# Performance work log

Measured on AMD Instinct MI355X. Metric: run time of the kernel, lower is better.

## Reference

```python
import jax, jax.numpy as jnp
import numpy as np

N_EMBD = 768
N_HEAD = 8
HEAD_DIM = N_EMBD // N_HEAD


def setup_inputs() -> dict:
    key = jax.random.key(0)
    k1, k2, k3 = jax.random.split(key, 3)
    B, T, C = 8, 1024, N_EMBD
    x = jax.random.normal(k1, (B, T, C), dtype=jnp.float32)
    # nn.Linear(C, 3C, bias=False): store as [C, 3C] so y = x @ W
    W_attn = jax.random.normal(k2, (C, 3 * C), dtype=jnp.float32) * (1.0 / np.sqrt(C))
    W_proj = jax.random.normal(k3, (C, C), dtype=jnp.float32) * (1.0 / np.sqrt(C))
    return {"x": x, "W_attn": W_attn, "W_proj": W_proj}


def reference(x, W_attn, W_proj):
    B, T, C = x.shape
    qkv = x @ W_attn                      # [B,T,3C]
    q, k, v = jnp.split(qkv, 3, axis=2)
    # [B,T,C] -> [B,H,T,D]
    def heads(t):
        return t.reshape(B, T, N_HEAD, HEAD_DIM).transpose(0, 2, 1, 3)
    q, k, v = heads(q), heads(k), heads(v)
    scale = 1.0 / np.sqrt(HEAD_DIM)
    att = jnp.einsum('bhtd,bhsd->bhts', q, k) * scale  # [B,H,T,T]
    causal = jnp.tril(jnp.ones((T, T), dtype=bool))
    att = jnp.where(causal[None, None], att, -jnp.inf)
    att = jax.nn.softmax(att, axis=-1)
    y = jnp.einsum('bhts,bhsd->bhtd', att, v)          # [B,H,T,D]
    y = y.transpose(0, 2, 1, 3).reshape(B, T, C)
    return y @ W_proj
```

## Files before the change

kernel.cpp:

```cpp
#include <hip/hip_runtime.h>
#include <stdint.h>

#define Bz 8
#define Tz 1024
#define Cz 768
#define Hz 8
#define Dz 96
#define BHz 64
#define Kz 768

typedef __bf16 bf16x8 __attribute__((ext_vector_type(8)));
typedef unsigned short u16x8 __attribute__((ext_vector_type(8)));
typedef float f32x4 __attribute__((ext_vector_type(4)));

__device__ __forceinline__ unsigned short f2bf(float f) {
  union { float f; unsigned int u; } v; v.f = f;
  unsigned int u = v.u;
  return (unsigned short)((u + 0x7fffu + ((u >> 16) & 1u)) >> 16);
}

__device__ __forceinline__ unsigned int cvtpk(float a, float b) {
  unsigned int r;
  asm("v_cvt_pk_bf16_f32 %0, %1, %2" : "=v"(r) : "v"(a), "v"(b));
  return r;
}

#if defined(__has_builtin)
#if __has_builtin(__builtin_amdgcn_exp2f)
#define EXP2(x) __builtin_amdgcn_exp2f(x)
#endif
#endif
#ifndef EXP2
#define EXP2(x) __expf((x) * 0.6931471805599453f)
#endif

typedef const __attribute__((address_space(1))) void* gas_ptr;
typedef __attribute__((address_space(3))) void* las_ptr;
__device__ __forceinline__ void gl16(const void* g, void* l) {
  __builtin_amdgcn_global_load_lds((gas_ptr)g, (las_ptr)l, 16, 0, 0);
}

__global__ __launch_bounds__(256) void prep(const float* __restrict__ x,
                                            unsigned short* __restrict__ xb,
                                            const float* __restrict__ Wa,
                                            unsigned short* __restrict__ Wat,
                                            const float* __restrict__ Wp,
                                            unsigned short* __restrict__ Wpt) {
  __shared__ unsigned short t[64][72];
  const int bid = blockIdx.x;
  const int tid = threadIdx.x;
  if (bid < 6144) {
    int i = (bid * 256 + tid) * 4;
    float4 v = *(const float4*)(x + i);
    union { unsigned short s[4]; uint2 u; } o;
    o.s[0] = f2bf(v.x); o.s[1] = f2bf(v.y); o.s[2] = f2bf(v.z); o.s[3] = f2bf(v.w);
    *(uint2*)(xb + i) = o.u;
    return;
  }
  const float* in; unsigned short* out; int R, Cc, bx, by;
  if (bid < 6576) { int q = bid - 6144; in = Wa; out = Wat; R = 768; Cc = 2304; bx = (q % 36) * 64; by = (q / 36) * 64; }
  else            { int q = bid - 6576; in = Wp; out = Wpt; R = 768; Cc = 768;  bx = (q % 12) * 64; by = (q / 12) * 64; }
#pragma unroll
  for (int i = 0; i < 16; i++) {
    int idx = tid + i * 256;
    int r = idx >> 6, c = idx & 63;
    t[c][r] = f2bf(in[(by + r) * Cc + bx + c]);
  }
  __syncthreads();
#pragma unroll
  for (int i = 0; i < 16; i++) {
    int idx = tid + i * 256;
    int r = idx >> 6, c = idx & 63;
    out[(bx + r) * R + by + c] = t[r][c];
  }
}

template <int MODE>
__global__ __launch_bounds__(256)
void gemm128(const unsigned short* __restrict__ A,
             const unsigned short* __restrict__ Bt,
             unsigned short* __restrict__ obf,
             float* __restrict__ of32) {
  __shared__ unsigned short Asm[2][128 * 32];
  __shared__ unsigned short Bsm[2][128 * 32];
  const int tid = threadIdx.x;
  const int wave = tid >> 6, lane = tid & 63;
  const int quad = lane >> 4, l16 = lane & 15;
  const int bm = blockIdx.x, bn = blockIdx.y;
  const int wm = (wave >> 1) * 64, wn = (wave & 1) * 64;

  f32x4 zero = {0.f, 0.f, 0.f, 0.f};
  f32x4 acc[4][4];
#pragma unroll
  for (int i = 0; i < 4; i++)
#pragma unroll
    for (int j = 0; j < 4; j++) acc[i][j] = zero;

  const int sch = (lane & 3) ^ ((lane >> 3) & 3);
  const unsigned short* Agp = A + (size_t)(bm * 128 + wave * 16 + (lane >> 2)) * Kz + sch * 8;
  const unsigned short* Bgp = Bt + (size_t)(bn * 128 + wave * 16 + (lane >> 2)) * Kz + sch * 8;
  const int ldst = (wave * 16) * 32;

#pragma unroll
  for (int g = 0; g < 2; g++) {
    gl16(Agp + g * 64 * Kz, &Asm[0][g * 2048 + ldst]);
    gl16(Bgp + g * 64 * Kz, &Bsm[0][g * 2048 + ldst]);
  }
  __syncthreads();

  const int rc = (quad ^ ((l16 >> 1) & 3)) << 3;
  int cur = 0;
  for (int t = 0; t < Kz / 32; t++) {
    if (t + 1 < Kz / 32) {
      const int kn = (t + 1) * 32;
#pragma unroll
      for (int g = 0; g < 2; g++) {
        gl16(Agp + g * 64 * Kz + kn, &Asm[cur ^ 1][g * 2048 + ldst]);
        gl16(Bgp + g * 64 * Kz + kn, &Bsm[cur ^ 1][g * 2048 + ldst]);
      }
    }
    bf16x8 af[4], bfr[4];
#pragma unroll
    for (int mi = 0; mi < 4; mi++)
      af[mi] = *(const bf16x8*)&Asm[cur][(wm + mi * 16 + l16) * 32 + rc];
#pragma unroll
    for (int ni = 0; ni < 4; ni++)
      bfr[ni] = *(const bf16x8*)&Bsm[cur][(wn + ni * 16 + l16) * 32 + rc];
#pragma unroll
    for (int mi = 0; mi < 4; mi++)
#pragma unroll
      for (int ni = 0; ni < 4; ni++)
        acc[mi][ni] = __builtin_amdgcn_mfma_f32_16x16x32_bf16(af[mi], bfr[ni], acc[mi][ni], 0, 0, 0);
    __syncthreads();
    cur ^= 1;
  }

#pragma unroll
  for (int mi = 0; mi < 4; mi++) {
    int row = bm * 128 + wm + mi * 16 + quad * 4;
    if (MODE == 0) {
      int b = row >> 10;
      int t = row & 1023;
#pragma unroll
      for (int ni = 0; ni < 4; ni++) {
        int col = bn * 128 + wn + ni * 16 + l16;
        int which = col / 768;
        int cc = col - which * 768;
        int h = cc / 96;
        int d = cc - h * 96;
        if (which == 2) {
          int tp = (t & ~31) | (((t >> 2) & 3) << 3) | (((t >> 4) & 1) << 2) | (t & 3);
          int base = ((2 * 64 + b * 8 + h) * 96 + d) * 1024 + tp;
          union { unsigned short s[4]; uint2 u; } o;
#pragma unroll
          for (int r = 0; r < 4; r++) o.s[r] = f2bf(acc[mi][ni][r]);
          *(uint2*)(obf + base) = o.u;
        } else {
          int base = ((which * 64 + b * 8 + h) * 1024 + t) * 96 + d;
#pragma unroll
          for (int r = 0; r < 4; r++) obf[base + r * 96] = f2bf(acc[mi][ni][r]);
        }
      }
    } else {
#pragma unroll
      for (int ni = 0; ni < 4; ni++) {
        int col = bn * 128 + wn + ni * 16 + l16;
#pragma unroll
        for (int r = 0; r < 4; r++) of32[(row + r) * 768 + col] = acc[mi][ni][r];
      }
    }
  }
}

__global__ __launch_bounds__(256, 4)
void attn(const unsigned short* __restrict__ qkv, unsigned short* __restrict__ y) {
  const int bh = blockIdx.x;
  const int by = blockIdx.y;
  const int q0 = (15 - by) * 64;
  const int tid = threadIdx.x;
  const int wave = tid >> 6, lane = tid & 63;
  const int quad = lane >> 4, l16 = lane & 15;
  const int qw0 = q0 + wave * 16;
  const int b = bh >> 3, h = bh & 7;

  const unsigned short* Qh = qkv + bh * Tz * Dz;
  const unsigned short* Kh = qkv + (BHz + bh) * Tz * Dz;
  const unsigned short* Vt = qkv + 2 * BHz * Tz * Dz + bh * Dz * Tz;

  __shared__ unsigned short Vsm[96 * 128];

  bf16x8 aq[3];
#pragma unroll
  for (int kd = 0; kd < 3; kd++)
    aq[kd] = *(const bf16x8*)(Qh + (qw0 + l16) * Dz + kd * 32 + quad * 8);

  f32x4 zero = {0.f, 0.f, 0.f, 0.f};
  f32x4 acc_o[6];
#pragma unroll
  for (int i = 0; i < 6; i++) acc_o[i] = zero;
  const float NEG = -__builtin_inff();
  float lrow = 0.f;
  const float cs = 0.14724538519872735f;
  const int t_abs = qw0 + l16;

  const int vrow = wave * 24 + (lane >> 4);
  const int vch = lane & 15;

  const int s_last = (q0 >> 7) << 7;
  for (int s0 = 0; s0 <= s_last; s0 += 128) {
    __syncthreads();
#pragma unroll
    for (int g = 0; g < 6; g++) {
      const int row = vrow + g * 4;
      gl16(Vt + row * Tz + s0 + ((vch ^ (row & 7)) << 3),
           &Vsm[(wave * 24 + g * 4) * 128]);
    }

    const int srem = qw0 + 15 - s0;
    const int nlim = min(7, srem >> 4);
    const int klim = min(3, srem >> 5);

    f32x4 sacc[8];
#pragma unroll
    for (int ni = 0; ni < 8; ni++) {
      if (ni <= nlim) {
        sacc[ni] = zero;
#pragma unroll
        for (int kd = 0; kd < 3; kd++) {
          bf16x8 bk = *(const bf16x8*)(Kh + (s0 + ni * 16 + l16) * Dz + kd * 32 + quad * 8);
          sacc[ni] = __builtin_amdgcn_mfma_f32_16x16x32_bf16(bk, aq[kd], sacc[ni], 0, 0, 0);
        }
      }
    }

#pragma unroll
    for (int ni = 0; ni < 8; ni++) {
      if (ni <= nlim && s0 + ni * 16 + 15 > qw0) {
        const int s_base = s0 + ni * 16 + quad * 4;
#pragma unroll
        for (int r = 0; r < 4; r++)
          if (s_base + r > t_abs) sacc[ni][r] = NEG;
      }
    }

    float rs[4] = {0.f, 0.f, 0.f, 0.f};
    unsigned int pk[8][2];
#pragma unroll
    for (int ni = 0; ni < 8; ni++) {
      if (ni <= nlim) {
        float p0 = EXP2(sacc[ni][0] * cs);
        float p1 = EXP2(sacc[ni][1] * cs);
        float p2 = EXP2(sacc[ni][2] * cs);
        float p3 = EXP2(sacc[ni][3] * cs);
        rs[0] += p0; rs[1] += p1; rs[2] += p2; rs[3] += p3;
        pk[ni][0] = cvtpk(p0, p1);
        pk[ni][1] = cvtpk(p2, p3);
      } else {
        pk[ni][0] = 0u; pk[ni][1] = 0u;
      }
    }
    lrow += (rs[0] + rs[1]) + (rs[2] + rs[3]);

    __syncthreads();

#pragma unroll
    for (int kc = 0; kc < 4; kc++) {
      if (kc <= klim) {
        union { unsigned int w[4]; bf16x8 v; } ap;
        ap.w[0] = pk[2 * kc][0];
        ap.w[1] = pk[2 * kc][1];
        ap.w[2] = pk[2 * kc + 1][0];
        ap.w[3] = pk[2 * kc + 1][1];
#pragma unroll
        for (int di = 0; di < 6; di++) {
          bf16x8 bv = *(const bf16x8*)&Vsm[(di * 16 + l16) * 128 +
                                           (((kc * 4 + quad) ^ (l16 & 7)) << 3)];
          acc_o[di] = __builtin_amdgcn_mfma_f32_16x16x32_bf16(ap.v, bv, acc_o[di], 0, 0, 0);
        }
      }
    }
  }

  lrow += __shfl_xor(lrow, 16);
  lrow += __shfl_xor(lrow, 32);
  float linv = 1.f / lrow;
  float lv[4];
#pragma unroll
  for (int r = 0; r < 4; r++) lv[r] = __shfl(linv, quad * 4 + r);
#pragma unroll
  for (int r = 0; r < 4; r++) {
    int t = qw0 + quad * 4 + r;
#pragma unroll
    for (int di = 0; di < 6; di++) {
      int d = di * 16 + l16;
      y[(b * Tz + t) * Cz + h * Dz + d] = f2bf(acc_o[di][r] * lv[r]);
    }
  }
}

#define OFF_XB   0u
#define OFF_WAT  12582912u
#define OFF_WPT  16121856u
#define OFF_QKV  17301504u
#define OFF_Y    55050240u

extern "C" void kernel_launch(void* const* d_in, const int* in_sizes, int n_in,
                              void* d_out, int out_size, void* d_ws, size_t ws_size,
                              hipStream_t stream) {
  const float* x  = (const float*)d_in[0];
  const float* Wa = (const float*)d_in[1];
  const float* Wp = (const float*)d_in[2];
  float* out = (float*)d_out;
  uint8_t* ws = (uint8_t*)d_ws;
  unsigned short* xb  = (unsigned short*)(ws + OFF_XB);
  unsigned short* Wat = (unsigned short*)(ws + OFF_WAT);
  unsigned short* Wpt = (unsigned short*)(ws + OFF_WPT);
  unsigned short* qkv = (unsigned short*)(ws + OFF_QKV);
  unsigned short* y   = (unsigned short*)(ws + OFF_Y);

  prep<<<6720, 256, 0, stream>>>(x, xb, Wa, Wat, Wp, Wpt);
  gemm128<0><<<dim3(64, 18), 256, 0, stream>>>(xb, Wat, qkv, nullptr);
  attn<<<dim3(64, 16), 256, 0, stream>>>(qkv, y);
  gemm128<1><<<dim3(64, 6), 256, 0, stream>>>(y, Wpt, nullptr, out);
}
```

Before: 198.7 us.

## Fuse x bf16 conversion into QKV GEMM, shrink output GEMM tile, reorder attention blocks

The QKV GEMM now reads fp32 x directly, converts it to bf16 in registers and stores it into swizzled LDS. This removes the separate conversion pass and its 12 MB intermediate buffer. The output projection GEMM moves to a 64-row tile, doubling the grid to 768 blocks for better CU fill. Attention query blocks are dispatched in an interleaved order so long and short causal rows mix across the grid. The cost is that every QKV block column re-reads and re-converts x in fp32 (18 times), which adds global traffic and register use.

```diff
diff --git a/kernel.cpp b/kernel.cpp
--- a/kernel.cpp
+++ b/kernel.cpp
@@ -40,26 +40,16 @@
   __builtin_amdgcn_global_load_lds((gas_ptr)g, (las_ptr)l, 16, 0, 0);
 }
 
-__global__ __launch_bounds__(256) void prep(const float* __restrict__ x,
-                                            unsigned short* __restrict__ xb,
-                                            const float* __restrict__ Wa,
+__global__ __launch_bounds__(256) void prep(const float* __restrict__ Wa,
                                             unsigned short* __restrict__ Wat,
                                             const float* __restrict__ Wp,
                                             unsigned short* __restrict__ Wpt) {
   __shared__ unsigned short t[64][72];
   const int bid = blockIdx.x;
   const int tid = threadIdx.x;
-  if (bid < 6144) {
-    int i = (bid * 256 + tid) * 4;
-    float4 v = *(const float4*)(x + i);
-    union { unsigned short s[4]; uint2 u; } o;
-    o.s[0] = f2bf(v.x); o.s[1] = f2bf(v.y); o.s[2] = f2bf(v.z); o.s[3] = f2bf(v.w);
-    *(uint2*)(xb + i) = o.u;
-    return;
-  }
   const float* in; unsigned short* out; int R, Cc, bx, by;
-  if (bid < 6576) { int q = bid - 6144; in = Wa; out = Wat; R = 768; Cc = 2304; bx = (q % 36) * 64; by = (q / 36) * 64; }
-  else            { int q = bid - 6576; in = Wp; out = Wpt; R = 768; Cc = 768;  bx = (q % 12) * 64; by = (q / 12) * 64; }
+  if (bid < 432) { int q = bid;       in = Wa; out = Wat; R = 768; Cc = 2304; bx = (q % 36) * 64; by = (q / 36) * 64; }
+  else           { int q = bid - 432; in = Wp; out = Wpt; R = 768; Cc = 768;  bx = (q % 12) * 64; by = (q / 12) * 64; }
 #pragma unroll
   for (int i = 0; i < 16; i++) {
     int idx = tid + i * 256;
@@ -75,12 +65,10 @@
   }
 }
 
-template <int MODE>
 __global__ __launch_bounds__(256)
-void gemm128(const unsigned short* __restrict__ A,
-             const unsigned short* __restrict__ Bt,
-             unsigned short* __restrict__ obf,
-             float* __restrict__ of32) {
+void gemm_qkv(const float* __restrict__ x,
+              const unsigned short* __restrict__ Bt,
+              unsigned short* __restrict__ obf) {
   __shared__ unsigned short Asm[2][128 * 32];
   __shared__ unsigned short Bsm[2][128 * 32];
   const int tid = threadIdx.x;
@@ -96,16 +84,115 @@
 #pragma unroll
     for (int j = 0; j < 4; j++) acc[i][j] = zero;
 
+  const int ar = tid >> 1, ah = tid & 1;
+  const float* xg = x + (size_t)(bm * 128 + ar) * Kz + ah * 16;
+  const int s4 = (ar >> 1) & 3;
+  const int ca = ((2 * ah) ^ s4) << 3;
+  const int cb = ((2 * ah + 1) ^ s4) << 3;
+
   const int sch = (lane & 3) ^ ((lane >> 3) & 3);
-  const unsigned short* Agp = A + (size_t)(bm * 128 + wave * 16 + (lane >> 2)) * Kz + sch * 8;
   const unsigned short* Bgp = Bt + (size_t)(bn * 128 + wave * 16 + (lane >> 2)) * Kz + sch * 8;
   const int ldst = (wave * 16) * 32;
 
-#pragma unroll
-  for (int g = 0; g < 2; g++) {
-    gl16(Agp + g * 64 * Kz, &Asm[0][g * 2048 + ldst]);
-    gl16(Bgp + g * 64 * Kz, &Bsm[0][g * 2048 + ldst]);
-  }
+  float4 xv0, xv1, xv2, xv3;
+#define LOADX(K) { xv0 = *(const float4*)(xg + (K));      xv1 = *(const float4*)(xg + (K) + 4); \
+                   xv2 = *(const float4*)(xg + (K) + 8);  xv3 = *(const float4*)(xg + (K) + 12); }
+#define STOREA(B) { uint4 da = { cvtpk(xv0.x, xv0.y), cvtpk(xv0.z, xv0.w),                      \
+                                 cvtpk(xv1.x, xv1.y), cvtpk(xv1.z, xv1.w) };                    \
+                    uint4 db = { cvtpk(xv2.x, xv2.y), cvtpk(xv2.z, xv2.w),                      \
+                                 cvtpk(xv3.x, xv3.y), cvtpk(xv3.z, xv3.w) };                    \
+                    *(uint4*)&Asm[B][ar * 32 + ca] = da;                                        \
+                    *(uint4*)&Asm[B][ar * 32 + cb] = db; }
+
+  LOADX(0);
+#pragma unroll
+  for (int g = 0; g < 2; g++) gl16(Bgp + g * 64 * Kz, &Bsm[0][g * 2048 + ldst]);
+  STOREA(0);
+  __syncthreads();
+
+  const int rc = (quad ^ ((l16 >> 1) & 3)) << 3;
+  int cur = 0;
+  for (int t = 0; t < Kz / 32; t++) {
+    const int nxt = (t + 1) * 32;
+    if (t + 1 < Kz / 32) {
+      LOADX(nxt);
+#pragma unroll
+      for (int g = 0; g < 2; g++) gl16(Bgp + g * 64 * Kz + nxt, &Bsm[cur ^ 1][g * 2048 + ldst]);
+    }
+    bf16x8 af[4], bfr[4];
+#pragma unroll
+    for (int mi = 0; mi < 4; mi++)
+      af[mi] = *(const bf16x8*)&Asm[cur][(wm + mi * 16 + l16) * 32 + rc];
+#pragma unroll
+    for (int ni = 0; ni < 4; ni++)
+      bfr[ni] = *(const bf16x8*)&Bsm[cur][(wn + ni * 16 + l16) * 32 + rc];
+#pragma unroll
+    for (int mi = 0; mi < 4; mi++)
+#pragma unroll
+      for (int ni = 0; ni < 4; ni++)
+        acc[mi][ni] = __builtin_amdgcn_mfma_f32_16x16x32_bf16(af[mi], bfr[ni], acc[mi][ni], 0, 0, 0);
+    if (t + 1 < Kz / 32) STOREA(cur ^ 1);
+    __syncthreads();
+    cur ^= 1;
+  }
+
+#pragma unroll
+  for (int mi = 0; mi < 4; mi++) {
+    int row = bm * 128 + wm + mi * 16 + quad * 4;
+    int b = row >> 10;
+    int t = row & 1023;
+#pragma unroll
+    for (int ni = 0; ni < 4; ni++) {
+      int col = bn * 128 + wn + ni * 16 + l16;
+      int which = col / 768;
+      int cc = col - which * 768;
+      int h = cc / 96;
+      int d = cc - h * 96;
+      if (which == 2) {
+        int tp = (t & ~31) | (((t >> 2) & 3) << 3) | (((t >> 4) & 1) << 2) | (t & 3);
+        int base = ((2 * 64 + b * 8 + h) * 96 + d) * 1024 + tp;
+        union { unsigned short s[4]; uint2 u; } o;
+#pragma unroll
+        for (int r = 0; r < 4; r++) o.s[r] = f2bf(acc[mi][ni][r]);
+        *(uint2*)(obf + base) = o.u;
+      } else {
+        int base = ((which * 64 + b * 8 + h) * 1024 + t) * 96 + d;
+#pragma unroll
+        for (int r = 0; r < 4; r++) obf[base + r * 96] = f2bf(acc[mi][ni][r]);
+      }
+    }
+  }
+#undef LOADX
+#undef STOREA
+}
+
+__global__ __launch_bounds__(256)
+void gemm_out(const unsigned short* __restrict__ A,
+              const unsigned short* __restrict__ Bt,
+              float* __restrict__ of32) {
+  __shared__ unsigned short Asm[2][64 * 32];
+  __shared__ unsigned short Bsm[2][128 * 32];
+  const int tid = threadIdx.x;
+  const int wave = tid >> 6, lane = tid & 63;
+  const int quad = lane >> 4, l16 = lane & 15;
+  const int bm = blockIdx.x, bn = blockIdx.y;
+  const int wm = (wave >> 1) * 32, wn = (wave & 1) * 64;
+
+  f32x4 zero = {0.f, 0.f, 0.f, 0.f};
+  f32x4 acc[2][4];
+#pragma unroll
+  for (int i = 0; i < 2; i++)
+#pragma unroll
+    for (int j = 0; j < 4; j++) acc[i][j] = zero;
+
+  const int sch = (lane & 3) ^ ((lane >> 3) & 3);
+  const unsigned short* Agp = A + (size_t)(bm * 64 + wave * 16 + (lane >> 2)) * Kz + sch * 8;
+  const unsigned short* Bgp = Bt + (size_t)(bn * 128 + wave * 16 + (lane >> 2)) * Kz + sch * 8;
+  const int ldst = (wave * 16) * 32;
+
+  gl16(Agp, &Asm[0][ldst]);
+#pragma unroll
+  for (int g = 0; g < 2; g++) gl16(Bgp + g * 64 * Kz, &Bsm[0][g * 2048 + ldst]);
   __syncthreads();
 
   const int rc = (quad ^ ((l16 >> 1) & 3)) << 3;
@@ -113,21 +200,19 @@
   for (int t = 0; t < Kz / 32; t++) {
     if (t + 1 < Kz / 32) {
       const int kn = (t + 1) * 32;
-#pragma unroll
-      for (int g = 0; g < 2; g++) {
-        gl16(Agp + g * 64 * Kz + kn, &Asm[cur ^ 1][g * 2048 + ldst]);
-        gl16(Bgp + g * 64 * Kz + kn, &Bsm[cur ^ 1][g * 2048 + ldst]);
-      }
-    }
-    bf16x8 af[4], bfr[4];
-#pragma unroll
-    for (int mi = 0; mi < 4; mi++)
+      gl16(Agp + kn, &Asm[cur ^ 1][ldst]);
+#pragma unroll
+      for (int g = 0; g < 2; g++) gl16(Bgp + g * 64 * Kz + kn, &Bsm[cur ^ 1][g * 2048 + ldst]);
+    }
+    bf16x8 af[2], bfr[4];
+#pragma unroll
+    for (int mi = 0; mi < 2; mi++)
       af[mi] = *(const bf16x8*)&Asm[cur][(wm + mi * 16 + l16) * 32 + rc];
 #pragma unroll
     for (int ni = 0; ni < 4; ni++)
       bfr[ni] = *(const bf16x8*)&Bsm[cur][(wn + ni * 16 + l16) * 32 + rc];
 #pragma unroll
-    for (int mi = 0; mi < 4; mi++)
+    for (int mi = 0; mi < 2; mi++)
 #pragma unroll
       for (int ni = 0; ni < 4; ni++)
         acc[mi][ni] = __builtin_amdgcn_mfma_f32_16x16x32_bf16(af[mi], bfr[ni], acc[mi][ni], 0, 0, 0);
@@ -136,38 +221,13 @@
   }
 
 #pragma unroll
-  for (int mi = 0; mi < 4; mi++) {
-    int row = bm * 128 + wm + mi * 16 + quad * 4;
-    if (MODE == 0) {
-      int b = row >> 10;
-      int t = row & 1023;
-#pragma unroll
-      for (int ni = 0; ni < 4; ni++) {
-        int col = bn * 128 + wn + ni * 16 + l16;
-        int which = col / 768;
-        int cc = col - which * 768;
-        int h = cc / 96;
-        int d = cc - h * 96;
-        if (which == 2) {
-          int tp = (t & ~31) | (((t >> 2) & 3) << 3) | (((t >> 4) & 1) << 2) | (t & 3);
-          int base = ((2 * 64 + b * 8 + h) * 96 + d) * 1024 + tp;
-          union { unsigned short s[4]; uint2 u; } o;
-#pragma unroll
-          for (int r = 0; r < 4; r++) o.s[r] = f2bf(acc[mi][ni][r]);
-          *(uint2*)(obf + base) = o.u;
-        } else {
-          int base = ((which * 64 + b * 8 + h) * 1024 + t) * 96 + d;
-#pragma unroll
-          for (int r = 0; r < 4; r++) obf[base + r * 96] = f2bf(acc[mi][ni][r]);
-        }
-      }
-    } else {
-#pragma unroll
-      for (int ni = 0; ni < 4; ni++) {
-        int col = bn * 128 + wn + ni * 16 + l16;
-#pragma unroll
-        for (int r = 0; r < 4; r++) of32[(row + r) * 768 + col] = acc[mi][ni][r];
-      }
+  for (int mi = 0; mi < 2; mi++) {
+    int row = bm * 64 + wm + mi * 16 + quad * 4;
+#pragma unroll
+    for (int ni = 0; ni < 4; ni++) {
+      int col = bn * 128 + wn + ni * 16 + l16;
+#pragma unroll
+      for (int r = 0; r < 4; r++) of32[(row + r) * 768 + col] = acc[mi][ni][r];
     }
   }
 }
@@ -176,7 +236,10 @@
 void attn(const unsigned short* __restrict__ qkv, unsigned short* __restrict__ y) {
   const int bh = blockIdx.x;
   const int by = blockIdx.y;
-  const int q0 = (15 - by) * 64;
+  const int gcl = by & 3, kcl = by >> 2;
+  const int j = (kcl == 0) ? (15 - gcl) : (kcl == 1) ? (8 + gcl)
+              : (kcl == 2) ? (4 + gcl) : (3 - gcl);
+  const int q0 = j * 64;
   const int tid = threadIdx.x;
   const int wave = tid >> 6, lane = tid & 63;
   const int quad = lane >> 4, l16 = lane & 15;
@@ -298,11 +361,10 @@
   }
 }
 
-#define OFF_XB   0u
-#define OFF_WAT  12582912u
-#define OFF_WPT  16121856u
-#define OFF_QKV  17301504u
-#define OFF_Y    55050240u
+#define OFF_WAT  0u
+#define OFF_WPT  3538944u
+#define OFF_QKV  4718592u
+#define OFF_Y    42467328u
 
 extern "C" void kernel_launch(void* const* d_in, const int* in_sizes, int n_in,
                               void* d_out, int out_size, void* d_ws, size_t ws_size,
@@ -312,14 +374,13 @@
   const float* Wp = (const float*)d_in[2];
   float* out = (float*)d_out;
   uint8_t* ws = (uint8_t*)d_ws;
-  unsigned short* xb  = (unsigned short*)(ws + OFF_XB);
   unsigned short* Wat = (unsigned short*)(ws + OFF_WAT);
   unsigned short* Wpt = (unsigned short*)(ws + OFF_WPT);
   unsigned short* qkv = (unsigned short*)(ws + OFF_QKV);
   unsigned short* y   = (unsigned short*)(ws + OFF_Y);
 
-  prep<<<6720, 256, 0, stream>>>(x, xb, Wa, Wat, Wp, Wpt);
-  gemm128<0><<<dim3(64, 18), 256, 0, stream>>>(xb, Wat, qkv, nullptr);
+  prep<<<576, 256, 0, stream>>>(Wa, Wat, Wp, Wpt);
+  gemm_qkv<<<dim3(64, 18), 256, 0, stream>>>(x, Wat, qkv);
   attn<<<dim3(64, 16), 256, 0, stream>>>(qkv, y);
-  gemm128<1><<<dim3(64, 6), 256, 0, stream>>>(y, Wpt, nullptr, out);
-}
+  gemm_out<<<dim3(128, 6), 256, 0, stream>>>(y, Wpt, out);
+}
```

New measurement: 209.6 us. 1.05x slower.
